# Kernel tuning notes

Hardware: AMD Instinct MI355X
Metric: run time of the kernel (lower is better)

Reference implementation:

```python
import jax, jax.numpy as jnp
import numpy as np

DIM = 512
HEADS = 8
HEAD_DIM = DIM // HEADS
WIN = 3
N = WIN * WIN  # 9 tokens per window
HID = 4 * DIM
B = 8192
SCALE = HEAD_DIM ** -0.5
EPS = 1e-5


def _relative_position_index():
    coords = np.stack(np.meshgrid(np.arange(WIN), np.arange(WIN), indexing='ij'))  # (2,W,W)
    flat = coords.reshape(2, -1)  # (2, N)
    rel = flat[:, :, None] - flat[:, None, :]  # (2, N, N)
    rel = rel.transpose(1, 2, 0).copy()  # (N, N, 2)
    rel[:, :, 0] += WIN - 1
    rel[:, :, 1] += WIN - 1
    rel[:, :, 0] *= 2 * WIN - 1
    return rel.sum(-1)  # (N, N) int

REL_IDX = jnp.asarray(_relative_position_index())


def _layernorm(x, g, b):
    mu = jnp.mean(x, axis=-1, keepdims=True)
    var = jnp.mean(jnp.square(x - mu), axis=-1, keepdims=True)
    return (x - mu) * jax.lax.rsqrt(var + EPS) * g + b


def setup_inputs() -> dict:
    key = jax.random.key(0)
    ks = jax.random.split(key, 16)
    f32 = jnp.float32
    return {
        'x': jax.random.normal(ks[0], (B, N, DIM), f32),
        'gamma1': jnp.ones((DIM,), f32),
        'beta1': jnp.zeros((DIM,), f32),
        'w_qkv': jax.random.normal(ks[1], (3 * DIM, DIM), f32) * 0.02,
        'b_qkv': jnp.zeros((3 * DIM,), f32),
        'bias_table': jax.random.normal(ks[2], ((2 * WIN - 1) ** 2, HEADS), f32) * 0.02,
        'w_proj': jax.random.normal(ks[3], (DIM, DIM), f32) * 0.02,
        'b_proj': jnp.zeros((DIM,), f32),
        'gamma2': jnp.ones((DIM,), f32),
        'beta2': jnp.zeros((DIM,), f32),
        'w_fc1': jax.random.normal(ks[4], (HID, DIM), f32) * 0.02,
        'b_fc1': jnp.zeros((HID,), f32),
        'w_fc2': jax.random.normal(ks[5], (DIM, HID), f32) * 0.02,
        'b_fc2': jnp.zeros((DIM,), f32),
        'w_conv': jax.random.normal(ks[6], (DIM, 1, WIN, WIN), f32) * 0.02,
        'b_conv': jnp.zeros((DIM,), f32),
    }


def reference(x, gamma1, beta1, w_qkv, b_qkv, bias_table, w_proj, b_proj,
              gamma2, beta2, w_fc1, b_fc1, w_fc2, b_fc2, w_conv, b_conv):
    Bn, Nn, C = x.shape
    # --- window attention ---
    shortcut = x
    h = _layernorm(x, gamma1, beta1)
    qkv = h @ w_qkv.T + b_qkv  # (B, N, 3C)
    qkv = qkv.reshape(Bn, Nn, 3, HEADS, HEAD_DIM).transpose(2, 0, 3, 1, 4)  # (3,B,H,N,d)
    q, k, v = qkv[0] * SCALE, qkv[1], qkv[2]
    attn = jnp.einsum('bhnd,bhmd->bhnm', q, k)  # (B,H,N,N)
    rel_bias = bias_table[REL_IDX.reshape(-1)].reshape(Nn, Nn, HEADS).transpose(2, 0, 1)  # (H,N,N)
    attn = jax.nn.softmax(attn + rel_bias[None], axis=-1)
    out = jnp.einsum('bhnm,bhmd->bhnd', attn, v)  # (B,H,N,d)
    out = out.transpose(0, 2, 1, 3).reshape(Bn, Nn, C)
    out = out @ w_proj.T + b_proj
    x = shortcut + out
    # --- MLP ---
    h = _layernorm(x, gamma2, beta2)
    h = jax.nn.gelu(h @ w_fc1.T + b_fc1, approximate=False)
    h = h @ w_fc2.T + b_fc2
    x = x + h
    # --- depthwise 3x3 merge conv over the 3x3 grid (valid -> 1x1) ---
    x4 = x.transpose(0, 2, 1).reshape(Bn, C, WIN, WIN)  # (B,C,3,3)
    y = jnp.einsum('bchw,chw->bc', x4, w_conv[:, 0]) + b_conv  # (B,C)
    return y[:, None, :]  # (B,1,C)
```

## Files before the change

### kernel.cpp

```cpp
#include <hip/hip_runtime.h>


typedef short short8 __attribute__((ext_vector_type(8)));
typedef unsigned short ushort8 __attribute__((ext_vector_type(8)));
typedef float floatx4 __attribute__((ext_vector_type(4)));

static constexpr int R_TOT = 73728;

__device__ __forceinline__ unsigned short f2bf(float f) {
  union { float f; unsigned int u; } v; v.f = f;
  unsigned int r = v.u + 0x7FFFu + ((v.u >> 16) & 1u);
  return (unsigned short)(r >> 16);
}
__device__ __forceinline__ float bf2f(unsigned short u) {
  union { unsigned int u; float f; } v; v.u = ((unsigned int)u) << 16;
  return v.f;
}

__device__ __forceinline__ void gload_lds16(const void* g, void* l) {
  __builtin_amdgcn_global_load_lds(
      (const __attribute__((address_space(1))) unsigned int*)g,
      (__attribute__((address_space(3))) unsigned int*)l, 16, 0, 0);
}

#define FENCE asm volatile("" ::: "memory")
#define BAR do { FENCE; __builtin_amdgcn_s_barrier(); FENCE; } while (0)
#define WAITV0 asm volatile("s_waitcnt vmcnt(0)" ::: "memory")
#define WAITV4 asm volatile("s_waitcnt vmcnt(4)" ::: "memory")
#define WAITV8 asm volatile("s_waitcnt vmcnt(8)" ::: "memory")

__global__ __launch_bounds__(256)
void cvt4(const float* __restrict__ in, unsigned short* __restrict__ out) {
  int i = (blockIdx.x * 256 + threadIdx.x) * 4;
  floatx4 v = *(const floatx4*)(in + i);
  union { unsigned short s[4]; unsigned long long u; } pk;
  pk.s[0] = f2bf(v[0]); pk.s[1] = f2bf(v[1]); pk.s[2] = f2bf(v[2]); pk.s[3] = f2bf(v[3]);
  *(unsigned long long*)(out + i) = pk.u;
}

__global__ __launch_bounds__(256)
void ln_bf16(const float* __restrict__ in, const float* __restrict__ g,
             const float* __restrict__ b, unsigned short* __restrict__ out) {
  const int lane = threadIdx.x & 63;
  const int wid = threadIdx.x >> 6;
  const size_t row = (size_t)blockIdx.x * 4 + wid;
  const float* p = in + row * 512 + lane * 8;
  floatx4 v0 = *(const floatx4*)p;
  floatx4 v1 = *(const floatx4*)(p + 4);
  float s = v0[0] + v0[1] + v0[2] + v0[3] + v1[0] + v1[1] + v1[2] + v1[3];
  float ss = v0[0]*v0[0] + v0[1]*v0[1] + v0[2]*v0[2] + v0[3]*v0[3]
           + v1[0]*v1[0] + v1[1]*v1[1] + v1[2]*v1[2] + v1[3]*v1[3];
  #pragma unroll
  for (int m = 1; m < 64; m <<= 1) { s += __shfl_xor(s, m); ss += __shfl_xor(ss, m); }
  float mu = s * (1.f / 512.f);
  float var = ss * (1.f / 512.f) - mu * mu;
  float rs = rsqrtf(var + 1e-5f);
  const float* gp = g + lane * 8;
  const float* bp = b + lane * 8;
  floatx4 g0 = *(const floatx4*)gp, g1 = *(const floatx4*)(gp + 4);
  floatx4 b0 = *(const floatx4*)bp, b1 = *(const floatx4*)(bp + 4);
  ushort8 o;
  o[0] = f2bf((v0[0] - mu) * rs * g0[0] + b0[0]);
  o[1] = f2bf((v0[1] - mu) * rs * g0[1] + b0[1]);
  o[2] = f2bf((v0[2] - mu) * rs * g0[2] + b0[2]);
  o[3] = f2bf((v0[3] - mu) * rs * g0[3] + b0[3]);
  o[4] = f2bf((v1[0] - mu) * rs * g1[0] + b1[0]);
  o[5] = f2bf((v1[1] - mu) * rs * g1[1] + b1[1]);
  o[6] = f2bf((v1[2] - mu) * rs * g1[2] + b1[2]);
  o[7] = f2bf((v1[3] - mu) * rs * g1[3] + b1[3]);
  *(ushort8*)(out + row * 512 + lane * 8) = o;
}


#define STAGE_A(d, qq, tk) do { \
  gload_lds16(Ap + (rowB + (qq)*64 + rowU) * (size_t)K + (tk) + kofsU, \
              sm + (d)*32768 + (qq)*16384 + wid*1024); \
  gload_lds16(Ap + (rowB + 128 + (qq)*64 + rowU) * (size_t)K + (tk) + kofsU, \
              sm + (d)*32768 + (qq)*16384 + 8192 + wid*1024); \
} while (0)

#define STAGE_B(d, hb, tk) do { \
  gload_lds16(Wp + (colB + (wid>>2)*64 + (hb)*32 + colU) * (size_t)K + (tk) + kofsU, \
              sm + 65536 + (d)*32768 + (hb)*16384 + wid*1024); \
  gload_lds16(Wp + (colB + (2 + (wid>>2))*64 + (hb)*32 + colU) * (size_t)K + (tk) + kofsU, \
              sm + 65536 + (d)*32768 + (hb)*16384 + 8192 + wid*1024); \
} while (0)

#define LOAD_A(d, qq) do { \
  _Pragma("unroll") \
  for (int fl = 0; fl < 4; ++fl) { \
    aF[fl][0] = *(const short8*)(sm + (d)*32768 + (qq)*16384 + wm*8192 + (fl*2+0)*1024 + laneRD); \
    aF[fl][1] = *(const short8*)(sm + (d)*32768 + (qq)*16384 + wm*8192 + (fl*2+1)*1024 + laneRD); \
  } \
} while (0)

#define LOAD_B(d, hb, BF) do { \
  _Pragma("unroll") \
  for (int nl = 0; nl < 2; ++nl) { \
    BF[nl][0] = *(const short8*)(sm + 65536 + (d)*32768 + (hb)*16384 + wn*4096 + (nl*2+0)*1024 + laneRD); \
    BF[nl][1] = *(const short8*)(sm + 65536 + (d)*32768 + (hb)*16384 + wn*4096 + (nl*2+1)*1024 + laneRD); \
  } \
} while (0)

#define MMQ(qa, hb, BF) do { \
  __builtin_amdgcn_s_setprio(1); \
  _Pragma("unroll") \
  for (int fl = 0; fl < 4; ++fl) \
    _Pragma("unroll") \
    for (int nl = 0; nl < 2; ++nl) { \
      acc[(qa)*4+fl][(hb)*2+nl] = __builtin_amdgcn_mfma_f32_16x16x32_bf16(aF[fl][0], BF[nl][0], acc[(qa)*4+fl][(hb)*2+nl], 0, 0, 0); \
      acc[(qa)*4+fl][(hb)*2+nl] = __builtin_amdgcn_mfma_f32_16x16x32_bf16(aF[fl][1], BF[nl][1], acc[(qa)*4+fl][(hb)*2+nl], 0, 0, 0); \
    } \
  __builtin_amdgcn_s_setprio(0); \
} while (0)

template <int EPI>
__global__ __launch_bounds__(512, 2)
void gemm8p(const unsigned short* __restrict__ Ap,
            const unsigned short* __restrict__ Wp,
            const float* __restrict__ bias,
            const float* __restrict__ resid,
            unsigned short* __restrict__ outb,
            float* __restrict__ outf,
            int K, int Nn, int ntn) {
  __shared__ __align__(16) char sm[131072];

  const int t = threadIdx.x;
  const int l = t & 63;
  const int wid = t >> 6;
  const int wm = wid >> 2;
  const int wn = wid & 3;

  const int nwg = gridDim.x;
  const int orig = blockIdx.x;
  const int q8 = nwg >> 3, r8 = nwg & 7;
  const int xcd = orig & 7, idx = orig >> 3;
  const int wg = (xcd < r8 ? xcd * (q8 + 1) : r8 * (q8 + 1) + (xcd - r8) * q8) + idx;
  const int tm = wg / ntn, tn = wg % ntn;
  const size_t rowB = (size_t)tm * 256;
  const size_t colB = (size_t)tn * 256;

  const int rowU = (wid >> 1) * 16 + (l >> 2);
  const int colU = ((wid >> 1) & 1) * 16 + (l >> 2);
  const int kofsU = (wid & 1) * 32 + (((l & 3) ^ ((l >> 4) & 3)) * 8);
  const int laneRD = (l & 15) * 64 + (((l >> 4) ^ ((l >> 2) & 3)) * 16);

  floatx4 acc[8][4];
  #pragma unroll
  for (int m = 0; m < 8; ++m)
    #pragma unroll
    for (int n = 0; n < 4; ++n)
      acc[m][n] = (floatx4){0.f, 0.f, 0.f, 0.f};

  short8 aF[4][2], bF0[2][2], bF1[2][2];

  STAGE_A(0, 0, 0);  STAGE_A(0, 1, 0);  STAGE_B(0, 0, 0);  STAGE_B(0, 1, 0);
  STAGE_A(1, 0, 64); STAGE_A(1, 1, 64); STAGE_B(1, 0, 64); STAGE_B(1, 1, 64);
  WAITV8; BAR;

  const int NI = K >> 7;
  for (int i = 0; i < NI; ++i) {
    const int tk1 = i * 128 + 64;
    const int tk2 = i * 128 + 128;
    const int tk3 = i * 128 + 192;
    const bool pre = (i > 0);
    const bool nxt = (i < NI - 1);

    LOAD_A(0, 0); LOAD_B(0, 0, bF0);
    if (pre) STAGE_A(1, 1, tk1);
    BAR; MMQ(0, 0, bF0); BAR;
    LOAD_B(0, 1, bF1);
    if (pre) STAGE_B(1, 0, tk1);
    BAR; MMQ(0, 1, bF1); BAR;
    LOAD_A(0, 1);
    if (nxt) STAGE_A(0, 0, tk2);
    BAR; MMQ(1, 1, bF1); BAR;
    if (nxt) STAGE_B(0, 1, tk2);
    BAR; MMQ(1, 0, bF0);
    if (nxt) { WAITV4; } else { WAITV0; }
    BAR;
    LOAD_A(1, 0); LOAD_B(1, 0, bF0);
    if (nxt) STAGE_A(0, 1, tk2);
    BAR; MMQ(0, 0, bF0); BAR;
    LOAD_B(1, 1, bF1);
    if (nxt) STAGE_B(0, 0, tk2);
    BAR; MMQ(0, 1, bF1); BAR;
    LOAD_A(1, 1);
    if (nxt) STAGE_A(1, 0, tk3);
    BAR; MMQ(1, 1, bF1); BAR;
    if (nxt) STAGE_B(1, 1, tk3);
    BAR; MMQ(1, 0, bF0);
    if (nxt) { WAITV4; }
    BAR;
  }
  FENCE;

  #pragma unroll
  for (int mi = 0; mi < 8; ++mi) {
    #pragma unroll
    for (int ni = 0; ni < 4; ++ni) {
      const int rr = (int)rowB + wm * 128 + (mi >> 2) * 64 + (mi & 3) * 16 + (l >> 4) * 4;
      const int cc = (int)colB + wn * 64 + (ni >> 1) * 32 + (ni & 1) * 16 + (l & 15);
      const float bs = bias[cc];
      #pragma unroll
      for (int j = 0; j < 4; ++j) {
        float v = acc[mi][ni][j] + bs;
        if (EPI == 1) v = 0.5f * v * (1.0f + erff(v * 0.70710678118654752f));
        if (EPI == 2) {
          v += resid[(size_t)(rr + j) * Nn + cc];
          outf[(size_t)(rr + j) * Nn + cc] = v;
        } else {
          outb[(size_t)(rr + j) * Nn + cc] = f2bf(v);
        }
      }
    }
  }
}

__global__ __launch_bounds__(256)
void attn9(const unsigned short* __restrict__ qkv,
           const float* __restrict__ bias_table,
           unsigned short* __restrict__ out) {
  __shared__ float qL[4][9][64];
  __shared__ float kL[4][9][64];
  __shared__ float vL[4][9][64];
  __shared__ float sL[4][9][10];

  const int lane = threadIdx.x & 63;
  const int wid = threadIdx.x >> 6;
  const int bh = blockIdx.x * 4 + wid;
  const int b = bh >> 3;
  const int h = bh & 7;

  const size_t base = (size_t)b * 9 * 1536 + h * 64 + lane;
  #pragma unroll
  for (int i = 0; i < 9; ++i) {
    qL[wid][i][lane] = bf2f(qkv[base + i * 1536]) * 0.125f;
    kL[wid][i][lane] = bf2f(qkv[base + i * 1536 + 512]);
    vL[wid][i][lane] = bf2f(qkv[base + i * 1536 + 1024]);
  }
  __syncthreads();

  #pragma unroll
  for (int p = 0; p < 2; ++p) {
    int pair = lane + p * 64;
    if (pair < 81) {
      int i = pair / 9, j = pair % 9;
      const floatx4* qi = (const floatx4*)qL[wid][i];
      const floatx4* kj = (const floatx4*)kL[wid][j];
      float dot = 0.f;
      #pragma unroll
      for (int d = 0; d < 16; ++d) {
        floatx4 a = qi[d], c = kj[d];
        dot += a[0]*c[0] + a[1]*c[1] + a[2]*c[2] + a[3]*c[3];
      }
      int dy = i / 3 - j / 3 + 2;
      int dx = i % 3 - j % 3 + 2;
      dot += bias_table[(dy * 5 + dx) * 8 + h];
      sL[wid][i][j] = dot;
    }
  }
  __syncthreads();

  if (lane < 9) {
    float m = -1e30f;
    #pragma unroll
    for (int j = 0; j < 9; ++j) m = fmaxf(m, sL[wid][lane][j]);
    float e[9], sum = 0.f;
    #pragma unroll
    for (int j = 0; j < 9; ++j) { e[j] = __expf(sL[wid][lane][j] - m); sum += e[j]; }
    float inv = 1.f / sum;
    #pragma unroll
    for (int j = 0; j < 9; ++j) sL[wid][lane][j] = e[j] * inv;
  }
  __syncthreads();

  const size_t obase = (size_t)b * 9 * 512 + h * 64 + lane;
  #pragma unroll
  for (int i = 0; i < 9; ++i) {
    float a = 0.f;
    #pragma unroll
    for (int j = 0; j < 9; ++j) a += sL[wid][i][j] * vL[wid][j][lane];
    out[obase + i * 512] = f2bf(a);
  }
}

__global__ __launch_bounds__(256)
void dwconv9(const float* __restrict__ x2, const float* __restrict__ wc,
             const float* __restrict__ bc, float* __restrict__ out) {
  int idx = blockIdx.x * 256 + threadIdx.x;
  int c = idx & 511;
  int b = idx >> 9;
  const float* xp = x2 + (size_t)b * 9 * 512 + c;
  float acc = bc[c];
  #pragma unroll
  for (int t = 0; t < 9; ++t) acc += xp[t * 512] * wc[c * 9 + t];
  out[idx] = acc;
}

extern "C" void kernel_launch(void* const* d_in, const int* in_sizes, int n_in,
                              void* d_out, int out_size, void* d_ws, size_t ws_size,
                              hipStream_t stream) {
  const float* x      = (const float*)d_in[0];
  const float* gamma1 = (const float*)d_in[1];
  const float* beta1  = (const float*)d_in[2];
  const float* w_qkv  = (const float*)d_in[3];
  const float* b_qkv  = (const float*)d_in[4];
  const float* bias_t = (const float*)d_in[5];
  const float* w_proj = (const float*)d_in[6];
  const float* b_proj = (const float*)d_in[7];
  const float* gamma2 = (const float*)d_in[8];
  const float* beta2  = (const float*)d_in[9];
  const float* w_fc1  = (const float*)d_in[10];
  const float* b_fc1  = (const float*)d_in[11];
  const float* w_fc2  = (const float*)d_in[12];
  const float* b_fc2  = (const float*)d_in[13];
  const float* w_conv = (const float*)d_in[14];
  const float* b_conv = (const float*)d_in[15];
  float* out = (float*)d_out;

  static const int cand[6] = {73728, 36864, 18432, 9216, 4608, 2304};
  int M_C = 2304;
  for (int i = 0; i < 6; ++i) {
    size_t need = 6291456ull + (size_t)cand[i] * 10240ull;
    if (need <= ws_size) { M_C = cand[i]; break; }
  }
  const int nChunks = R_TOT / M_C;
  const int winC = M_C / 9;

  char* ws = (char*)d_ws;
  unsigned short* wqkvb  = (unsigned short*)(ws);
  unsigned short* wprojb = (unsigned short*)(ws + 1572864);
  unsigned short* wfc1b  = (unsigned short*)(ws + 2097152);
  unsigned short* wfc2b  = (unsigned short*)(ws + 4194304);
  char* base = ws + 6291456;
  const size_t szHB  = (size_t)M_C * 1024;
  const size_t szQKV = (size_t)M_C * 3072;
  const size_t szX1  = (size_t)M_C * 2048;
  unsigned short* hb   = (unsigned short*)base;
  unsigned short* aob  = hb;
  unsigned short* qkvb = (unsigned short*)(base + szHB);
  unsigned short* h2b  = qkvb;
  float* x2            = (float*)(base + szHB + szHB);
  float* x1            = (float*)(base + szHB + szQKV);
  unsigned short* gb   = (unsigned short*)(base + szHB + szQKV + szX1);

  cvt4<<<768, 256, 0, stream>>>(w_qkv, wqkvb);
  cvt4<<<256, 256, 0, stream>>>(w_proj, wprojb);
  cvt4<<<1024, 256, 0, stream>>>(w_fc1, wfc1b);
  cvt4<<<1024, 256, 0, stream>>>(w_fc2, wfc2b);

  const int mt256 = M_C / 256;
  for (int ch = 0; ch < nChunks; ++ch) {
    const size_t rOff = (size_t)ch * M_C;
    const float* xC = x + rOff * 512;
    float* outC = out + (size_t)ch * winC * 512;

    ln_bf16<<<M_C / 4, 256, 0, stream>>>(xC, gamma1, beta1, hb);
    gemm8p<0><<<dim3(mt256 * 6), 512, 0, stream>>>(hb, wqkvb, b_qkv, nullptr, qkvb, nullptr, 512, 1536, 6);
    attn9<<<winC * 2, 256, 0, stream>>>(qkvb, bias_t, aob);
    gemm8p<2><<<dim3(mt256 * 2), 512, 0, stream>>>(aob, wprojb, b_proj, xC, nullptr, x1, 512, 512, 2);
    ln_bf16<<<M_C / 4, 256, 0, stream>>>(x1, gamma2, beta2, h2b);
    gemm8p<1><<<dim3(mt256 * 8), 512, 0, stream>>>(h2b, wfc1b, b_fc1, nullptr, gb, nullptr, 512, 2048, 8);
    gemm8p<2><<<dim3(mt256 * 2), 512, 0, stream>>>(gb, wfc2b, b_fc2, x1, nullptr, x2, 2048, 512, 2);
    dwconv9<<<winC * 2, 256, 0, stream>>>(x2, w_conv, b_conv, outC);
  }
}
```

Baseline: 1.372 ms.

## Restructure GEMM LDS tile layout with 128-byte rows and batch the prefetch stages

```diff
diff --git a/kernel.cpp b/kernel.cpp
--- a/kernel.cpp
+++ b/kernel.cpp
@@ -72,44 +72,37 @@
 }
 
 
-#define STAGE_A(d, qq, tk) do { \
-  gload_lds16(Ap + (rowB + (qq)*64 + rowU) * (size_t)K + (tk) + kofsU, \
-              sm + (d)*32768 + (qq)*16384 + wid*1024); \
-  gload_lds16(Ap + (rowB + 128 + (qq)*64 + rowU) * (size_t)K + (tk) + kofsU, \
-              sm + (d)*32768 + (qq)*16384 + 8192 + wid*1024); \
-} while (0)
-
-#define STAGE_B(d, hb, tk) do { \
-  gload_lds16(Wp + (colB + (wid>>2)*64 + (hb)*32 + colU) * (size_t)K + (tk) + kofsU, \
-              sm + 65536 + (d)*32768 + (hb)*16384 + wid*1024); \
-  gload_lds16(Wp + (colB + (2 + (wid>>2))*64 + (hb)*32 + colU) * (size_t)K + (tk) + kofsU, \
-              sm + 65536 + (d)*32768 + (hb)*16384 + 8192 + wid*1024); \
-} while (0)
-
-#define LOAD_A(d, qq) do { \
+#define STAGE_AU(d, u, tk) \
+  gload_lds16(Ap + (rowB + (u)*64 + srow) * (size_t)K + (tk) + skofs, \
+              sm + (d)*65536 + (u)*8192 + wid*1024)
+#define STAGE_BU(d, u, tk) \
+  gload_lds16(Wp + (colB + (u)*64 + srow) * (size_t)K + (tk) + skofs, \
+              sm + (d)*65536 + 32768 + (u)*8192 + wid*1024)
+
+#define LOAD_A(d, mh) do { \
   _Pragma("unroll") \
   for (int fl = 0; fl < 4; ++fl) { \
-    aF[fl][0] = *(const short8*)(sm + (d)*32768 + (qq)*16384 + wm*8192 + (fl*2+0)*1024 + laneRD); \
-    aF[fl][1] = *(const short8*)(sm + (d)*32768 + (qq)*16384 + wm*8192 + (fl*2+1)*1024 + laneRD); \
+    aF[fl][0] = *(const short8*)(sm + (d)*65536 + (wm*2+(mh))*8192 + fl*2048 + aoff0); \
+    aF[fl][1] = *(const short8*)(sm + (d)*65536 + (wm*2+(mh))*8192 + fl*2048 + aoff1); \
   } \
 } while (0)
 
-#define LOAD_B(d, hb, BF) do { \
+#define LOAD_B(d, nh, BF) do { \
   _Pragma("unroll") \
   for (int nl = 0; nl < 2; ++nl) { \
-    BF[nl][0] = *(const short8*)(sm + 65536 + (d)*32768 + (hb)*16384 + wn*4096 + (nl*2+0)*1024 + laneRD); \
-    BF[nl][1] = *(const short8*)(sm + 65536 + (d)*32768 + (hb)*16384 + wn*4096 + (nl*2+1)*1024 + laneRD); \
+    BF[nl][0] = *(const short8*)(sm + (d)*65536 + 32768 + wn*8192 + ((nh)*2+nl)*2048 + aoff0); \
+    BF[nl][1] = *(const short8*)(sm + (d)*65536 + 32768 + wn*8192 + ((nh)*2+nl)*2048 + aoff1); \
   } \
 } while (0)
 
-#define MMQ(qa, hb, BF) do { \
+#define MMQ(mh, nh, BF) do { \
   __builtin_amdgcn_s_setprio(1); \
   _Pragma("unroll") \
   for (int fl = 0; fl < 4; ++fl) \
     _Pragma("unroll") \
     for (int nl = 0; nl < 2; ++nl) { \
-      acc[(qa)*4+fl][(hb)*2+nl] = __builtin_amdgcn_mfma_f32_16x16x32_bf16(aF[fl][0], BF[nl][0], acc[(qa)*4+fl][(hb)*2+nl], 0, 0, 0); \
-      acc[(qa)*4+fl][(hb)*2+nl] = __builtin_amdgcn_mfma_f32_16x16x32_bf16(aF[fl][1], BF[nl][1], acc[(qa)*4+fl][(hb)*2+nl], 0, 0, 0); \
+      acc[(mh)*4+fl][(nh)*2+nl] = __builtin_amdgcn_mfma_f32_16x16x32_bf16(aF[fl][0], BF[nl][0], acc[(mh)*4+fl][(nh)*2+nl], 0, 0, 0); \
+      acc[(mh)*4+fl][(nh)*2+nl] = __builtin_amdgcn_mfma_f32_16x16x32_bf16(aF[fl][1], BF[nl][1], acc[(mh)*4+fl][(nh)*2+nl], 0, 0, 0); \
     } \
   __builtin_amdgcn_s_setprio(0); \
 } while (0)
@@ -140,10 +133,12 @@
   const size_t rowB = (size_t)tm * 256;
   const size_t colB = (size_t)tn * 256;
 
-  const int rowU = (wid >> 1) * 16 + (l >> 2);
-  const int colU = ((wid >> 1) & 1) * 16 + (l >> 2);
-  const int kofsU = (wid & 1) * 32 + (((l & 3) ^ ((l >> 4) & 3)) * 8);
-  const int laneRD = (l & 15) * 64 + (((l >> 4) ^ ((l >> 2) & 3)) * 16);
+  const int srow = wid * 8 + (l >> 3);
+  const int skofs = ((l & 7) ^ (l >> 3)) * 8;
+
+  const int arow = l & 15;
+  const int aoff0 = arow * 128 + (((l >> 4) + 0) ^ (arow & 7)) * 16;
+  const int aoff1 = arow * 128 + (((l >> 4) + 4) ^ (arow & 7)) * 16;
 
   floatx4 acc[8][4];
   #pragma unroll
@@ -154,43 +149,53 @@
 
   short8 aF[4][2], bF0[2][2], bF1[2][2];
 
-  STAGE_A(0, 0, 0);  STAGE_A(0, 1, 0);  STAGE_B(0, 0, 0);  STAGE_B(0, 1, 0);
-  STAGE_A(1, 0, 64); STAGE_A(1, 1, 64); STAGE_B(1, 0, 64); STAGE_B(1, 1, 64);
+  #pragma unroll
+  for (int u = 0; u < 4; ++u) STAGE_AU(0, u, 0);
+  #pragma unroll
+  for (int u = 0; u < 4; ++u) STAGE_BU(0, u, 0);
+  #pragma unroll
+  for (int u = 0; u < 4; ++u) STAGE_AU(1, u, 64);
+  #pragma unroll
+  for (int u = 0; u < 4; ++u) STAGE_BU(1, u, 64);
   WAITV8; BAR;
 
-  const int NI = K >> 7;
-  for (int i = 0; i < NI; ++i) {
-    const int tk1 = i * 128 + 64;
-    const int tk2 = i * 128 + 128;
-    const int tk3 = i * 128 + 192;
-    const bool pre = (i > 0);
-    const bool nxt = (i < NI - 1);
+  const int NI2 = K >> 7;
+  for (int i = 0; i < NI2; ++i) {
+    const int k2 = i * 128 + 128;
+    const int k3 = i * 128 + 192;
+    const bool nxt = (i < NI2 - 1);
 
     LOAD_A(0, 0); LOAD_B(0, 0, bF0);
-    if (pre) STAGE_A(1, 1, tk1);
     BAR; MMQ(0, 0, bF0); BAR;
     LOAD_B(0, 1, bF1);
-    if (pre) STAGE_B(1, 0, tk1);
     BAR; MMQ(0, 1, bF1); BAR;
     LOAD_A(0, 1);
-    if (nxt) STAGE_A(0, 0, tk2);
     BAR; MMQ(1, 1, bF1); BAR;
-    if (nxt) STAGE_B(0, 1, tk2);
+    if (nxt) {
+      #pragma unroll
+      for (int u = 0; u < 4; ++u) STAGE_AU(0, u, k2);
+    }
     BAR; MMQ(1, 0, bF0);
     if (nxt) { WAITV4; } else { WAITV0; }
     BAR;
     LOAD_A(1, 0); LOAD_B(1, 0, bF0);
-    if (nxt) STAGE_A(0, 1, tk2);
+    if (nxt) {
+      #pragma unroll
+      for (int u = 0; u < 4; ++u) STAGE_BU(0, u, k2);
+    }
     BAR; MMQ(0, 0, bF0); BAR;
     LOAD_B(1, 1, bF1);
-    if (nxt) STAGE_B(0, 0, tk2);
     BAR; MMQ(0, 1, bF1); BAR;
     LOAD_A(1, 1);
-    if (nxt) STAGE_A(1, 0, tk3);
     BAR; MMQ(1, 1, bF1); BAR;
-    if (nxt) STAGE_B(1, 1, tk3);
+    if (nxt) {
+      #pragma unroll
+      for (int u = 0; u < 4; ++u) STAGE_AU(1, u, k3);
+      #pragma unroll
+      for (int u = 0; u < 4; ++u) STAGE_BU(1, u, k3);
+    }
     BAR; MMQ(1, 0, bF0);
-    if (nxt) { WAITV4; }
+    if (nxt) { WAITV8; }
     BAR;
   }
   FENCE;
@@ -199,8 +204,8 @@
   for (int mi = 0; mi < 8; ++mi) {
     #pragma unroll
     for (int ni = 0; ni < 4; ++ni) {
-      const int rr = (int)rowB + wm * 128 + (mi >> 2) * 64 + (mi & 3) * 16 + (l >> 4) * 4;
-      const int cc = (int)colB + wn * 64 + (ni >> 1) * 32 + (ni & 1) * 16 + (l & 15);
+      const int rr = (int)rowB + wm * 128 + mi * 16 + (l >> 4) * 4;
+      const int cc = (int)colB + wn * 64 + ni * 16 + (l & 15);
       const float bs = bias[cc];
       #pragma unroll
       for (int j = 0; j < 4; ++j) {
```

Result: no change. 1.372 ms (-0.0%).
